# Optimization experiments

Measured on AMD Instinct MI355X. Metric: run time of the kernel, lower is better.

## Reference

```python
import jax, jax.numpy as jnp
import numpy as np

NUM_HEADS = 8
STRIDE = 1
PAD = 1


def _conv(x, w, stride=STRIDE, pad=PAD):
    return jax.lax.conv_general_dilated(
        x, w, (stride, stride), [(pad, pad), (pad, pad)],
        dimension_numbers=("NCHW", "OIHW", "NCHW"))


def setup_inputs() -> dict:
    key = jax.random.key(0)
    ks = jax.random.split(key, 5)
    B, C, H, W = 8, 64, 56, 56
    nh = NUM_HEADS
    x = jax.random.normal(ks[0], (B, C, H, W), dtype=jnp.float32)
    # Conv weights, small init for numerical stability
    Wq = jax.random.normal(ks[1], (C * nh, C, 3, 3), dtype=jnp.float32) * 0.05
    Wk = jax.random.normal(ks[2], (C * nh, C, 3, 3), dtype=jnp.float32) * 0.05
    Wv = jax.random.normal(ks[3], (C * nh, C, 3, 3), dtype=jnp.float32) * 0.05
    Wu = jax.random.normal(ks[4], (C, C * nh, 1, 1), dtype=jnp.float32) * 0.05
    return {"x": x, "Wq": Wq, "Wk": Wk, "Wv": Wv, "Wu": Wu}


def reference(x, Wq, Wk, Wv, Wu):
    B, C, H, W = x.shape
    nh = NUM_HEADS
    # projections: [B, nh*C, H, W] -> [B, nh, C, H, W] -> [B, C, nh, H, W]
    def proj(w):
        y = _conv(x, w).reshape(B, nh, C, H, W)
        return jnp.transpose(y, (0, 2, 1, 3, 4))
    q = proj(Wq)  # [B, C, nh, H, W]
    k = proj(Wk)
    v = proj(Wv)
    scale = 1.0 / np.sqrt(C * nh).astype(np.float32)
    # contract over heads axis ('n'), attend over channel axis: [B, Cq, H, W, Ck]
    scores = jnp.einsum("bqnhw,bknhw->bqhwk", q, k) * scale
    attn = jax.nn.softmax(scores, axis=-1)
    # attended: [B, Cq, nh, H, W]
    attended = jnp.einsum("bqhwk,bknhw->bqnhw", attn, v)
    out = _conv(attended.reshape(B, C * nh, H, W), Wu, stride=1, pad=0)
    return jax.nn.relu(out)
```

## Files before the change

### kernel.cpp

```cpp
#include <hip/hip_runtime.h>
#include <hip/hip_bf16.h>

#define HW   56
#define CIN  64
#define OC   512
#define NPIX (HW * HW)
#define PEL  ((size_t)8 * NPIX * OC)

typedef unsigned short ushort_t;
typedef __attribute__((ext_vector_type(8))) short short8;
typedef __attribute__((ext_vector_type(4))) float floatx4;
typedef __attribute__((ext_vector_type(16))) float floatx16;

static __device__ __forceinline__ ushort_t f2bf(float f) {
  __hip_bfloat16 h = __float2bfloat16(f);
  return *(ushort_t*)&h;
}

#if __has_builtin(__builtin_amdgcn_exp2f)
#define EXP2F(x) __builtin_amdgcn_exp2f(x)
#else
#define EXP2F(x) exp2f(x)
#endif

__global__ __launch_bounds__(256)
void prep_kernel(const float* __restrict__ x, const float* __restrict__ W0,
                 const float* __restrict__ W1, const float* __restrict__ W2,
                 const float* __restrict__ Wu, ushort_t* __restrict__ xT,
                 ushort_t* __restrict__ Wb, ushort_t* __restrict__ WuP) {
  __shared__ ushort_t lx[CIN * HW];
  const int bid = blockIdx.x;
  const int tid = threadIdx.x;

  if (bid < 448) {
    const int h = bid % HW, b = bid / HW;
    for (int idx = tid; idx < CIN * HW; idx += 256) {
      int c = idx / HW, w = idx - c * HW;
      lx[idx] = f2bf(x[((size_t)(b * CIN + c) * HW + h) * HW + w]);
    }
    __syncthreads();
    ushort_t* dst = xT + ((size_t)(b * HW + h)) * HW * CIN;
    for (int i = tid; i < (CIN * HW) / 4; i += 256) {
      int e0 = i * 4;
      int w = e0 >> 6, c0 = e0 & 63;
      ushort4 o;
      o.x = lx[(c0 + 0) * HW + w];
      o.y = lx[(c0 + 1) * HW + w];
      o.z = lx[(c0 + 2) * HW + w];
      o.w = lx[(c0 + 3) * HW + w];
      ((ushort4*)dst)[i] = o;
    }
  } else if (bid < 832) {
    const int u = bid - 448;
    const int sel = u / 128;
    const int j = (u % 128) * 4 + (tid >> 6);
    const int cin = tid & 63;
    const float* W = sel == 0 ? W0 : (sel == 1 ? W1 : W2);
    ushort_t* Ds = Wb + (size_t)sel * 9 * OC * CIN;
    const int src = (sel < 2) ? ((j & 7) * 64 + (j >> 3)) : j;
    #pragma unroll
    for (int tap = 0; tap < 9; ++tap)
      Ds[((size_t)tap * OC + j) * CIN + cin] = f2bf(W[(size_t)src * 576 + cin * 9 + tap]);
  } else {
    const int el = (bid - 832) * 256 + tid;
    WuP[el] = f2bf(Wu[el]);
  }
}

#define XLS 72
#define XROW (58 * XLS)

__global__ __launch_bounds__(256, 2)
void conv3x3_qkv(const ushort_t* __restrict__ xT, const ushort_t* __restrict__ Wb,
                 ushort_t* __restrict__ yq) {
  __shared__ __align__(16) ushort_t xl[6 * XROW];

  const int tid  = threadIdx.x;
  const int lane = tid & 63;
  const int wv   = tid >> 6;
  const int g    = blockIdx.x;
  const int ob   = blockIdx.y;
  const int b    = blockIdx.z;
  const int h0   = g * 4;
  const int l31  = lane & 31;
  const int khi  = lane >> 5;

  int rowcol[7], rowv[7];
  #pragma unroll
  for (int t = 0; t < 7; ++t) {
    int p = t * 32 + l31;
    int row = p / HW, ww = p - row * HW;
    rowcol[t] = (row * 58 + ww) * XLS;
    rowv[t] = row;
  }

  const ushort_t* wb0 = Wb + ((size_t)(ob * 128 + wv * 32 + l31)) * CIN + khi * 8;

  for (int r = 0; r < 6; ++r) {
    int gh = h0 - 1 + r;
    const int sw = 2 * ((-r) & 3);
    if (gh >= 0 && gh < HW) {
      const uint4* src = (const uint4*)(xT + ((size_t)(b * HW + gh) * HW) * CIN);
      for (int idx = tid; idx < 448; idx += 256) {
        int w = idx >> 3, c8 = idx & 7;
        int col = 1 + w;
        int p8 = (c8 + sw) & 7;
        *(uint4*)&xl[(r * 58 + col) * XLS + p8 * 8] = src[idx];
      }
      if (tid < 16) {
        int col = (tid >> 3) ? 57 : 0, c8 = tid & 7;
        int p8 = (c8 + sw) & 7;
        *(uint4*)&xl[(r * 58 + col) * XLS + p8 * 8] = (uint4){0, 0, 0, 0};
      }
    } else {
      for (int idx = tid; idx < 464; idx += 256) {
        int col = idx >> 3, c8 = idx & 7;
        int p8 = (c8 + sw) & 7;
        *(uint4*)&xl[(r * 58 + col) * XLS + p8 * 8] = (uint4){0, 0, 0, 0};
      }
    }
  }

  short8 BfA[4], BfB[4];
  #pragma unroll
  for (int ck = 0; ck < 4; ++ck)
    BfA[ck] = *(const short8*)(wb0 + ck * 16);

  __syncthreads();

  #pragma unroll 1
  for (int s = 0; s < 3; ++s) {
    floatx16 acc[7];
    #pragma unroll
    for (int t = 0; t < 7; ++t) acc[t] = (floatx16)(0.0f);

    #pragma unroll
    for (int tap = 0; tap < 9; ++tap) {
      const int wtap = s * 9 + tap;
      if (wtap < 26) {
        #pragma unroll
        for (int ck = 0; ck < 4; ++ck)
          BfB[ck] = *(const short8*)(wb0 + (size_t)(wtap + 1) * (OC * CIN) + ck * 16);
      }
      const int kh = tap / 3, kw = tap - kh * 3;
      int baddr[7], b8[7];
      #pragma unroll
      for (int t = 0; t < 7; ++t) {
        baddr[t] = rowcol[t] + (kh * 58 + kw) * XLS;
        b8[t] = khi + 2 * ((-(rowv[t] + kh)) & 3);
      }
      #pragma unroll
      for (int ck = 0; ck < 4; ++ck) {
        #pragma unroll
        for (int t = 0; t < 7; ++t) {
          int chunk = (b8[t] + 2 * ck) & 7;
          short8 af = *(const short8*)&xl[baddr[t] + chunk * 8];
          acc[t] = __builtin_amdgcn_mfma_f32_32x32x16_bf16(af, BfA[ck], acc[t], 0, 0, 0);
        }
      }
      #pragma unroll
      for (int ck = 0; ck < 4; ++ck) BfA[ck] = BfB[ck];
    }

    ushort_t* y = yq + (size_t)s * PEL;
    const int oc = ob * 128 + wv * 32 + l31;
    #pragma unroll
    for (int t = 0; t < 7; ++t) {
      #pragma unroll
      for (int i = 0; i < 16; ++i) {
        int p = t * 32 + (i & 3) + 8 * (i >> 2) + 4 * khi;
        int row = p / HW, ww = p - row * HW;
        size_t pb = ((size_t)((b * HW + h0 + row) * HW + ww)) * OC;
        y[pb + oc] = f2bf(acc[t][i]);
      }
    }
  }
}

#define PST  72
#define A2ST 520

__global__ __launch_bounds__(256, 3)
void attn_kernel(const ushort_t* __restrict__ q, const ushort_t* __restrict__ k,
                 const ushort_t* __restrict__ v, const ushort_t* __restrict__ WuP,
                 float* __restrict__ out) {
  __shared__ __align__(16) ushort_t Pl[4][64 * PST];
  __shared__ __align__(16) ushort_t a2[16 * A2ST];

  const int tid  = threadIdx.x;
  const int lane = tid & 63;
  const int wv   = tid >> 6;
  const int l15  = lane & 15;
  const int quad = lane >> 4;
  const int p0   = blockIdx.x * 16;
  const int b    = blockIdx.y;
  const size_t ibase = ((size_t)b * NPIX + p0) * 512;

  ushort_t* Pw = &Pl[wv][0];
  const float scale2 = 0.063758723f;

  auto loadpix = [&](int plocal, short8 qf[4], short8 kf[4], short8 vf[2]) {
    const ushort_t* qp = q + ibase + (size_t)plocal * 512;
    const ushort_t* kp = k + ibase + (size_t)plocal * 512;
    const ushort_t* vp = v + ibase + (size_t)plocal * 512;
    #pragma unroll
    for (int nt = 0; nt < 4; ++nt)
      qf[nt] = *(const short8*)(qp + (nt * 16 + l15) * 8);
    #pragma unroll
    for (int mt = 0; mt < 4; ++mt) {
      kf[mt] = (short8){0, 0, 0, 0, 0, 0, 0, 0};
      if (quad == 0) kf[mt] = *(const short8*)(kp + (mt * 16 + l15) * 8);
    }
    #pragma unroll
    for (int ck = 0; ck < 2; ++ck)
      vf[ck] = *(const short8*)(vp + (l15 & 7) * 64 + ck * 32 + quad * 8);
  };

  short8 qf[4], kf[4], vf[2];
  loadpix(wv * 4, qf, kf, vf);

  #pragma unroll
  for (int i = 0; i < 4; ++i) {
    const int plocal = wv * 4 + i;
    short8 qn[4], kn[4], vn[2];
    if (i < 3) loadpix(plocal + 1, qn, kn, vn);

    floatx4 S[4][4];
    #pragma unroll
    for (int mt = 0; mt < 4; ++mt)
      #pragma unroll
      for (int nt = 0; nt < 4; ++nt) S[mt][nt] = (floatx4){0.f, 0.f, 0.f, 0.f};
    #pragma unroll
    for (int mt = 0; mt < 4; ++mt)
      #pragma unroll
      for (int nt = 0; nt < 4; ++nt)
        S[mt][nt] = __builtin_amdgcn_mfma_f32_16x16x32_bf16(kf[mt], qf[nt], S[mt][nt], 0, 0, 0);

    float inv[4];
    #pragma unroll
    for (int nt = 0; nt < 4; ++nt) {
      float e[4][4];
      #pragma unroll
      for (int mt = 0; mt < 4; ++mt)
        #pragma unroll
        for (int r = 0; r < 4; ++r)
          e[mt][r] = EXP2F(S[mt][nt][r] * scale2);
      float sm[4];
      #pragma unroll
      for (int mt = 0; mt < 4; ++mt)
        sm[mt] = (e[mt][0] + e[mt][1]) + (e[mt][2] + e[mt][3]);
      float sum = (sm[0] + sm[1]) + (sm[2] + sm[3]);
      sum += __shfl_xor(sum, 16);
      sum += __shfl_xor(sum, 32);
      inv[nt] = __builtin_amdgcn_rcpf(sum);
      #pragma unroll
      for (int mt = 0; mt < 4; ++mt) {
        ushort4 w4;
        w4.x = f2bf(e[mt][0]);
        w4.y = f2bf(e[mt][1]);
        w4.z = f2bf(e[mt][2]);
        w4.w = f2bf(e[mt][3]);
        *(ushort4*)&Pw[(nt * 16 + l15) * PST + mt * 16 + quad * 4] = w4;
      }
    }

    floatx4 T[4];
    #pragma unroll
    for (int nt = 0; nt < 4; ++nt) T[nt] = (floatx4){0.f, 0.f, 0.f, 0.f};
    #pragma unroll
    for (int ck = 0; ck < 2; ++ck) {
      #pragma unroll
      for (int nt = 0; nt < 4; ++nt) {
        short8 pf = *(const short8*)&Pw[(nt * 16 + l15) * PST + ck * 32 + quad * 8];
        T[nt] = __builtin_amdgcn_mfma_f32_16x16x32_bf16(vf[ck], pf, T[nt], 0, 0, 0);
      }
    }
    if (quad < 2) {
      #pragma unroll
      for (int nt = 0; nt < 4; ++nt) {
        ushort4 w4;
        w4.x = f2bf(T[nt][0] * inv[nt]);
        w4.y = f2bf(T[nt][1] * inv[nt]);
        w4.z = f2bf(T[nt][2] * inv[nt]);
        w4.w = f2bf(T[nt][3] * inv[nt]);
        *(ushort4*)&a2[plocal * A2ST + (nt * 16 + l15) * 8 + quad * 4] = w4;
      }
    }

    if (i < 3) {
      #pragma unroll
      for (int z = 0; z < 4; ++z) { qf[z] = qn[z]; kf[z] = kn[z]; }
      vf[0] = vn[0];
      vf[1] = vn[1];
    }
  }
  __syncthreads();

  floatx4 O = (floatx4){0.f, 0.f, 0.f, 0.f};
  #pragma unroll
  for (int ck = 0; ck < 16; ++ck) {
    short8 aw = *(const short8*)(WuP + (size_t)(wv * 16 + l15) * 512 + ck * 32 + quad * 8);
    short8 bw = *(const short8*)&a2[l15 * A2ST + ck * 32 + quad * 8];
    O = __builtin_amdgcn_mfma_f32_16x16x32_bf16(aw, bw, O, 0, 0, 0);
  }
  #pragma unroll
  for (int r = 0; r < 4; ++r) {
    int co = wv * 16 + quad * 4 + r;
    out[((size_t)b * 64 + co) * NPIX + p0 + l15] = fmaxf(O[r], 0.f);
  }
}

extern "C" void kernel_launch(void* const* d_in, const int* in_sizes, int n_in,
                              void* d_out, int out_size, void* d_ws, size_t ws_size,
                              hipStream_t stream) {
  const float* x  = (const float*)d_in[0];
  const float* Wq = (const float*)d_in[1];
  const float* Wk = (const float*)d_in[2];
  const float* Wv = (const float*)d_in[3];
  const float* Wu = (const float*)d_in[4];
  float* out = (float*)d_out;

  const size_t xT_elems = (size_t)8 * NPIX * CIN;
  const size_t w_elems  = (size_t)9 * OC * CIN;
  const size_t wu_elems = (size_t)64 * 512;
  ushort_t* xT  = (ushort_t*)d_ws;
  ushort_t* Wb  = xT + xT_elems;
  ushort_t* WuP = Wb + 3 * w_elems;
  ushort_t* q   = WuP + wu_elems;
  ushort_t* k   = q + PEL;
  ushort_t* v   = k + PEL;

  prep_kernel<<<960, 256, 0, stream>>>(x, Wq, Wk, Wv, Wu, xT, Wb, WuP);

  dim3 cgrid(14, 4, 8);
  conv3x3_qkv<<<cgrid, 256, 0, stream>>>(xT, Wb, q);

  attn_kernel<<<dim3(NPIX / 16, 8), 256, 0, stream>>>(q, k, v, WuP, out);
}
```

Baseline: 152.4 us.

## Split QKV conv across grid z and retile waves into 2x2 pixel/channel blocks

The three Q/K/V projections move from a serial loop inside each block to the grid z dimension, so the grid grows from 448 to 1344 blocks. Each block now reloads the input tile once per projection. Waves are retiled so each handles up to 4 pixel tiles by 64 output channels using two MFMA accumulators, sharing each A fragment across two B fragments. This cuts LDS reads per MFMA, but the wave that covers pixel tiles 4-7 only has three valid tiles, which leaves some imbalance.

Result: slower. 177.2 us (+16.3%).

```diff
diff --git a/kernel.cpp b/kernel.cpp
--- a/kernel.cpp
+++ b/kernel.cpp
@@ -80,21 +80,28 @@
   const int wv   = tid >> 6;
   const int g    = blockIdx.x;
   const int ob   = blockIdx.y;
-  const int b    = blockIdx.z;
+  const int z    = blockIdx.z;
+  const int b    = z & 7;
+  const int s    = z >> 3;
   const int h0   = g * 4;
   const int l31  = lane & 31;
   const int khi  = lane >> 5;
 
-  int rowcol[7], rowv[7];
-  #pragma unroll
-  for (int t = 0; t < 7; ++t) {
-    int p = t * 32 + l31;
+  const int th    = wv >> 1;
+  const int oh    = wv & 1;
+  const int tbase = th * 4;
+
+  int rowcol[4], rowv[4];
+  #pragma unroll
+  for (int t = 0; t < 4; ++t) {
+    int p = (tbase + t) * 32 + l31;
     int row = p / HW, ww = p - row * HW;
     rowcol[t] = (row * 58 + ww) * XLS;
     rowv[t] = row;
   }
 
-  const ushort_t* wb0 = Wb + ((size_t)(ob * 128 + wv * 32 + l31)) * CIN + khi * 8;
+  const ushort_t* wb0 = Wb + (size_t)s * 9 * OC * CIN +
+                        ((size_t)(ob * 128 + oh * 64 + l31)) * CIN + khi * 8;
 
   for (int r = 0; r < 6; ++r) {
     int gh = h0 - 1 + r;
@@ -121,57 +128,55 @@
     }
   }
 
-  short8 BfA[4], BfB[4];
-  #pragma unroll
-  for (int ck = 0; ck < 4; ++ck)
-    BfA[ck] = *(const short8*)(wb0 + ck * 16);
+  short8 Bc0 = *(const short8*)(wb0);
+  short8 Bc1 = *(const short8*)(wb0 + 32 * CIN);
+
+  floatx16 acc[4][2];
+  #pragma unroll
+  for (int t = 0; t < 4; ++t) {
+    acc[t][0] = (floatx16)(0.0f);
+    acc[t][1] = (floatx16)(0.0f);
+  }
 
   __syncthreads();
 
-  #pragma unroll 1
-  for (int s = 0; s < 3; ++s) {
-    floatx16 acc[7];
-    #pragma unroll
-    for (int t = 0; t < 7; ++t) acc[t] = (floatx16)(0.0f);
-
-    #pragma unroll
-    for (int tap = 0; tap < 9; ++tap) {
-      const int wtap = s * 9 + tap;
-      if (wtap < 26) {
-        #pragma unroll
-        for (int ck = 0; ck < 4; ++ck)
-          BfB[ck] = *(const short8*)(wb0 + (size_t)(wtap + 1) * (OC * CIN) + ck * 16);
-      }
-      const int kh = tap / 3, kw = tap - kh * 3;
-      int baddr[7], b8[7];
-      #pragma unroll
-      for (int t = 0; t < 7; ++t) {
-        baddr[t] = rowcol[t] + (kh * 58 + kw) * XLS;
-        b8[t] = khi + 2 * ((-(rowv[t] + kh)) & 3);
-      }
-      #pragma unroll
-      for (int ck = 0; ck < 4; ++ck) {
-        #pragma unroll
-        for (int t = 0; t < 7; ++t) {
-          int chunk = (b8[t] + 2 * ck) & 7;
-          short8 af = *(const short8*)&xl[baddr[t] + chunk * 8];
-          acc[t] = __builtin_amdgcn_mfma_f32_32x32x16_bf16(af, BfA[ck], acc[t], 0, 0, 0);
-        }
-      }
-      #pragma unroll
-      for (int ck = 0; ck < 4; ++ck) BfA[ck] = BfB[ck];
-    }
-
-    ushort_t* y = yq + (size_t)s * PEL;
-    const int oc = ob * 128 + wv * 32 + l31;
-    #pragma unroll
-    for (int t = 0; t < 7; ++t) {
+  #pragma unroll
+  for (int step = 0; step < 36; ++step) {
+    const int tap = step >> 2, ck = step & 3;
+    short8 Bn0, Bn1;
+    if (step < 35) {
+      const int ntap = (step + 1) >> 2, nck = (step + 1) & 3;
+      const size_t boff = (size_t)ntap * (OC * CIN) + nck * 16;
+      Bn0 = *(const short8*)(wb0 + boff);
+      Bn1 = *(const short8*)(wb0 + boff + 32 * CIN);
+    } else {
+      Bn0 = Bc0; Bn1 = Bc1;
+    }
+    const int kh = tap / 3, kw = tap - kh * 3;
+    #pragma unroll
+    for (int t = 0; t < 4; ++t) {
+      if (tbase + t < 7) {
+        int chunk = (khi + 2 * ((-(rowv[t] + kh)) & 3) + 2 * ck) & 7;
+        short8 af = *(const short8*)&xl[rowcol[t] + (kh * 58 + kw) * XLS + chunk * 8];
+        acc[t][0] = __builtin_amdgcn_mfma_f32_32x32x16_bf16(af, Bc0, acc[t][0], 0, 0, 0);
+        acc[t][1] = __builtin_amdgcn_mfma_f32_32x32x16_bf16(af, Bc1, acc[t][1], 0, 0, 0);
+      }
+    }
+    Bc0 = Bn0; Bc1 = Bn1;
+  }
+
+  ushort_t* y = yq + (size_t)s * PEL;
+  const int ocb = ob * 128 + oh * 64 + l31;
+  #pragma unroll
+  for (int t = 0; t < 4; ++t) {
+    if (tbase + t < 7) {
       #pragma unroll
       for (int i = 0; i < 16; ++i) {
-        int p = t * 32 + (i & 3) + 8 * (i >> 2) + 4 * khi;
+        int p = (tbase + t) * 32 + (i & 3) + 8 * (i >> 2) + 4 * khi;
         int row = p / HW, ww = p - row * HW;
         size_t pb = ((size_t)((b * HW + h0 + row) * HW + ww)) * OC;
-        y[pb + oc] = f2bf(acc[t][i]);
+        y[pb + ocb]      = f2bf(acc[t][0][i]);
+        y[pb + ocb + 32] = f2bf(acc[t][1][i]);
       }
     }
   }
@@ -332,7 +337,7 @@
 
   prep_kernel<<<960, 256, 0, stream>>>(x, Wq, Wk, Wv, Wu, xT, Wb, WuP);
 
-  dim3 cgrid(14, 4, 8);
+  dim3 cgrid(14, 4, 24);
   conv3x3_qkv<<<cgrid, 256, 0, stream>>>(xT, Wb, q);
 
   attn_kernel<<<dim3(NPIX / 16, 8), 256, 0, stream>>>(q, k, v, WuP, out);
```
